# Optimization experiments

Measured on AMD Instinct MI355X. Metric: run time of the kernel, lower is better.

Reference implementation:

```python
import jax, jax.numpy as jnp
import numpy as np


def conv2d(x, w, pad=0, groups=1, bias=None):
    out = jax.lax.conv_general_dilated(
        x, w, (1, 1), [(pad, pad), (pad, pad)],
        dimension_numbers=('NCHW', 'OIHW', 'NCHW'), feature_group_count=groups)
    return out if bias is None else out + bias[None, :, None, None]


def l2norm(t):
    # F.normalize(t, dim=-1): divide by max(||t||_2, 1e-12)
    return t / jnp.maximum(jnp.sqrt(jnp.sum(t * t, axis=-1, keepdims=True)), 1e-12)


def chan_attn(q, k, v, temp, heads):
    # transposed (channel) attention: contract over N=H*W, softmax over small channel dim
    b, _, h, w = v.shape
    n = h * w
    q = l2norm(q.reshape(b, heads, -1, n))
    k = l2norm(k.reshape(b, heads, -1, n))
    v = v.reshape(b, heads, -1, n)
    attn = jax.nn.softmax(jnp.einsum('bhdn,bhen->bhde', q, k) * temp, axis=-1)
    return jnp.einsum('bhde,bhen->bhdn', attn, v).reshape(b, -1, h, w)


def nearest_resize(x, H, W):
    # torch F.interpolate(mode='nearest'): idx = floor(i * in/out)
    hi, wi = x.shape[2], x.shape[3]
    iy = jnp.arange(H) * hi // H
    ix = jnp.arange(W) * wi // W
    return x[:, :, iy][:, :, :, ix]


def deform_conv(x, offsets, w, bias, k, pad, groups):
    # torchvision DeformConv2d, stride=1, dilation=1, offset layout [B, 2*k*k, H, W] as (dy, dx) pairs
    B, Cin, H, W = x.shape
    K2 = k * k
    off = offsets.reshape(B, K2, 2, H, W)
    ky, kx = jnp.meshgrid(jnp.arange(k), jnp.arange(k), indexing='ij')
    py = (jnp.arange(H)[None, None, :, None] - pad) + ky.reshape(1, K2, 1, 1) + off[:, :, 0]
    px = (jnp.arange(W)[None, None, None, :] - pad) + kx.reshape(1, K2, 1, 1) + off[:, :, 1]
    y0f = jnp.floor(py); x0f = jnp.floor(px)
    wy = (py - y0f)[:, None]  # [B,1,K2,H,W]
    wx = (px - x0f)[:, None]
    y0 = y0f.astype(jnp.int32); x0 = x0f.astype(jnp.int32)
    xf = x.reshape(B, Cin, H * W)

    def gather(yi, xi):
        valid = ((yi >= 0) & (yi < H) & (xi >= 0) & (xi < W)).astype(x.dtype)
        idx = (jnp.clip(yi, 0, H - 1) * W + jnp.clip(xi, 0, W - 1)).reshape(B, 1, -1)
        v = jnp.take_along_axis(xf, idx, axis=2).reshape(B, Cin, K2, H, W)
        return v * valid[:, None]

    s = (gather(y0, x0) * (1 - wy) * (1 - wx)
         + gather(y0, x0 + 1) * (1 - wy) * wx
         + gather(y0 + 1, x0) * wy * (1 - wx)
         + gather(y0 + 1, x0 + 1) * wy * wx)  # [B, Cin, K2, H, W]
    g = groups
    s = s.reshape(B, g, Cin // g, K2, H, W)
    wg = w.reshape(g, w.shape[0] // g, Cin // g, K2)
    out = jnp.einsum('bgckhw,gock->bgohw', s, wg).reshape(B, -1, H, W)
    return out + bias[None, :, None, None]


def scconv(x, w_k2, w_k3, w_k4):
    B, C, H, W = x.shape
    p = x.reshape(B, C, H // 2, 2, W // 2, 2).mean(axis=(3, 5))  # AvgPool2d(2,2)
    a = jax.nn.sigmoid(nearest_resize(conv2d(p, w_k2, pad=0), H, W))
    return conv2d(conv2d(x, w_k3, pad=1) * a, w_k4, pad=1)


def layernorm_c(x, g, b):
    # LayerNorm over channel dim of NCHW (applied as [B, HW, C] in the original)
    b_, c, h, w = x.shape
    t = x.reshape(b_, c, h * w).transpose(0, 2, 1)
    mu = t.mean(-1, keepdims=True)
    var = ((t - mu) ** 2).mean(-1, keepdims=True)
    t = (t - mu) / jnp.sqrt(var + 1e-5) * g + b
    return t.transpose(0, 2, 1).reshape(b_, c, h, w)


def _forward(x, y, temp, w_po, w_lp1, w_lp2, ln_g, ln_b, temp_in, w_qkv, w_qkvd,
             w_mproj, w_c3, w_k2, w_k3, w_k4, w_d3, b_d3, w_d5, b_d5, w_d7, b_d7,
             w_pw, b_pw):
    b, c, h, w = x.shape
    heads = 8
    # --- Multi_Receptive_Attentive_Prompts ---
    l1 = conv2d(x, w_lp1)
    l2 = conv2d(x, w_lp2, pad=1)
    xn = layernorm_c(x, ln_g, ln_b)
    qkv = conv2d(conv2d(xn, w_qkv), w_qkvd, pad=1, groups=c)
    qi, ki, vi = jnp.split(qkv, 3, axis=1)
    xg = x + conv2d(chan_attn(qi, ki, vi, temp_in, heads), w_mproj)
    prompt = conv2d(jnp.concatenate([l1, l2, xg], axis=1), w_c3, pad=1)
    # --- Temporal_Alignment ---
    offs = scconv(jnp.concatenate([x, y], axis=1), w_k2, w_k3, w_k4)  # [B,166,H,W]
    f3 = jax.nn.relu(deform_conv(x, offs[:, :18], w_d3, b_d3, 3, 1, 8))
    f5 = jax.nn.relu(deform_conv(x, offs[:, 18:68], w_d5, b_d5, 5, 2, 8))
    f7 = jax.nn.relu(deform_conv(x, offs[:, 68:166], w_d7, b_d7, 7, 3, 8))
    k_feat = conv2d(jnp.concatenate([f3, f5, f7], axis=1), w_pw, bias=b_pw)
    # --- prompted channel attention ---
    q_feat = jnp.concatenate([x, prompt], axis=1)  # 2c channels -> d_q = 2c/heads
    out = chan_attn(q_feat, k_feat, x, temp, heads)  # [B, 2c, H, W]
    return conv2d(out, w_po)


def setup_inputs() -> dict:
    key = jax.random.key(0)
    ks = jax.random.split(key, 16)
    C, B, H, W = 32, 2, 128, 128
    r = lambda k, shp: jax.random.normal(k, shp, dtype=jnp.float32) * 0.05
    return {
        'x': jax.random.normal(ks[0], (B, C, H, W), dtype=jnp.float32),
        'y': jax.random.normal(ks[1], (B, C, H, W), dtype=jnp.float32),
        'temp': jnp.ones((1, 8, 1, 1), jnp.float32),
        'w_po': r(ks[2], (C, 2 * C, 1, 1)),
        'w_lp1': r(ks[3], (C, C, 1, 1)),
        'w_lp2': r(ks[4], (C, C, 3, 3)),
        'ln_g': jnp.ones((C,), jnp.float32),
        'ln_b': jnp.zeros((C,), jnp.float32),
        'temp_in': jnp.ones((1, 8, 1, 1), jnp.float32),
        'w_qkv': r(ks[5], (3 * C, C, 1, 1)),
        'w_qkvd': r(ks[6], (3 * C, 3, 3, 3)),  # groups=C: in/groups = 3
        'w_mproj': r(ks[7], (C, C, 1, 1)),
        'w_c3': r(ks[8], (C, 3 * C, 3, 3)),
        'w_k2': r(ks[9], (166, 2 * C, 3, 3)),
        'w_k3': r(ks[10], (166, 2 * C, 3, 3)),
        'w_k4': r(ks[11], (166, 166, 3, 3)),
        'w_d3': r(ks[12], (C, C // 8, 3, 3)),
        'b_d3': jnp.zeros((C,), jnp.float32),
        'w_d5': r(ks[13], (C, C // 8, 5, 5)),
        'b_d5': jnp.zeros((C,), jnp.float32),
        'w_d7': r(ks[14], (C, C // 8, 7, 7)),
        'b_d7': jnp.zeros((C,), jnp.float32),
        'w_pw': r(ks[15], (C, 3 * C, 1, 1)),
        'b_pw': jnp.zeros((C,), jnp.float32),
    }


def reference(x, y, temp, w_po, w_lp1, w_lp2, ln_g, ln_b, temp_in, w_qkv, w_qkvd,
              w_mproj, w_c3, w_k2, w_k3, w_k4, w_d3, b_d3, w_d5, b_d5, w_d7, b_d7,
              w_pw, b_pw):
    return _forward(x, y, temp, w_po, w_lp1, w_lp2, ln_g, ln_b, temp_in, w_qkv,
                    w_qkvd, w_mproj, w_c3, w_k2, w_k3, w_k4, w_d3, b_d3, w_d5,
                    b_d5, w_d7, b_d7, w_pw, b_pw)
```

## Files before the change

kernel.cpp:

```cpp
#include <hip/hip_runtime.h>
#include <hip/hip_bf16.h>
#include <hip/hip_fp16.h>


constexpr int B = 2, C = 32, H = 128, W = 128, N = H * W;

using bh8   = __attribute__((ext_vector_type(8))) short;
using f32x4 = __attribute__((ext_vector_type(4))) float;

__device__ __forceinline__ ushort f2bf(float v) {
  __hip_bfloat16 h = __float2bfloat16(v);
  return *(ushort*)&h;
}
__device__ __forceinline__ float bf2f(ushort u) {
  union { unsigned int i; float f; } w; w.i = ((unsigned int)u) << 16; return w.f;
}

__global__ __launch_bounds__(256) void k_prep(const float* __restrict__ x,
                                              const float* __restrict__ y,
                                              const float* __restrict__ ln_g,
                                              const float* __restrict__ ln_b,
                                              float* __restrict__ cat2,
                                              ushort* __restrict__ xtb,
                                              ushort* __restrict__ cat2b,
                                              float* __restrict__ xn,
                                              ushort* __restrict__ poolb) {
  __shared__ float tile[C][257];
  const int b = blockIdx.y, n0 = blockIdx.x * 256, tid = threadIdx.x;
  const int n = n0 + tid;
  const int prow = blockIdx.x;
  for (int c = 0; c < C; c++) {
    float v = x[(size_t)(b * C + c) * N + n];
    tile[c][tid] = v;
    cat2[(size_t)(b * 64 + c) * N + n] = v;
  }
  __syncthreads();
  {
    float s = 0.f, ss = 0.f;
#pragma unroll
    for (int c = 0; c < C; c++) { const float v = tile[c][tid]; s += v; ss += v * v; }
    const float mu = s * (1.f / C);
    const float var = ss * (1.f / C) - mu * mu;
    const float inv = rsqrtf(var + 1e-5f);
#pragma unroll
    for (int c = 0; c < C; c++)
      xn[(size_t)(b * C + c) * N + n] = (tile[c][tid] - mu) * inv * ln_g[c] + ln_b[c];
  }
  for (int i = tid; i < C * 256; i += 256) {
    int c = i & 31, nl = i >> 5;
    const ushort bv = f2bf(tile[c][nl]);
    xtb[((size_t)b * N + n0 + nl) * 32 + c] = bv;
    cat2b[((size_t)b * N + n0 + nl) * 64 + c] = bv;
  }
  for (int i = tid; i < 2048; i += 256) {
    const int ox = i >> 5, c = i & 31;
    const float pv = 0.25f * (tile[c][2 * ox] + tile[c][2 * ox + 1]
                            + tile[c][128 + 2 * ox] + tile[c][128 + 2 * ox + 1]);
    poolb[((size_t)b * 4096 + prow * 64 + ox) * 64 + c] = f2bf(pv);
  }
  __syncthreads();
  for (int c = 0; c < C; c++) {
    float v = y[(size_t)(b * C + c) * N + n];
    tile[c][tid] = v;
    cat2[(size_t)(b * 64 + 32 + c) * N + n] = v;
  }
  __syncthreads();
  for (int i = tid; i < C * 256; i += 256) {
    int c = i & 31, nl = i >> 5;
    cat2b[((size_t)b * N + n0 + nl) * 64 + 32 + c] = f2bf(tile[c][nl]);
  }
  for (int i = tid; i < 2048; i += 256) {
    const int ox = i >> 5, c = i & 31;
    const float pv = 0.25f * (tile[c][2 * ox] + tile[c][2 * ox + 1]
                            + tile[c][128 + 2 * ox] + tile[c][128 + 2 * ox + 1]);
    poolb[((size_t)b * 4096 + prow * 64 + ox) * 64 + 32 + c] = f2bf(pv);
  }
}

struct WEnt { const float* src; ushort* dst; int cout_real, cin_real, kc32, total; };
struct WArgs { WEnt e[5]; };

__global__ __launch_bounds__(256) void k_wpack(WArgs a) {
  const WEnt en = a.e[blockIdx.y];
  const int tk = 9 * en.kc32;
  for (int i = blockIdx.x * 256 + threadIdx.x; i < en.total; i += gridDim.x * 256) {
    const int co = i / tk, rem = i - co * tk;
    const int t = rem / en.kc32, ci = rem - t * en.kc32;
    float v = 0.f;
    if (co < en.cout_real && ci < en.cin_real)
      v = en.src[((size_t)co * en.cin_real + ci) * 9 + t];
    en.dst[i] = f2bf(v);
  }
}

__global__ __launch_bounds__(256)
void k_conv3m(const ushort* __restrict__ xin, long in_bs, int in_cs, int ih, int iw,
              const ushort* __restrict__ wp, int kchunks, int cout_real,
              void* __restrict__ outp, long out_bs, int out_coff,
              int oh, int ow, int pad, int omode, int out_cs, int store_tot,
              const float* __restrict__ gatep) {
  __shared__ ushort smem[17408];
  ushort* xt = smem;
  const int tid = threadIdx.x, b = blockIdx.z;
  const int y0 = blockIdx.x * 2, co0 = blockIdx.y * 32;
  const int wv = tid >> 6, lane = tid & 63;
  const int row_sel = wv >> 1, col0 = (wv & 1) * 64;
  const int q = lane >> 4, n = lane & 15, q8 = q * 8;
  const int kc32 = kchunks * 32;
  const ushort* xb = xin + (size_t)b * in_bs;

  f32x4 acc[2][4];
#pragma unroll
  for (int mt = 0; mt < 2; mt++)
#pragma unroll
    for (int nb = 0; nb < 4; nb++) acc[mt][nb] = (f32x4){0.f, 0.f, 0.f, 0.f};

  for (int cc = 0; cc < kchunks; cc++) {
    __syncthreads();
    for (int i = tid; i < 2080; i += 256) {
      const int qq = i & 3, rc = i >> 2;
      const int r = rc / 130, c = rc - r * 130;
      const int yy = y0 - pad + r, xx = c - pad;
      bh8 v = {0, 0, 0, 0, 0, 0, 0, 0};
      if (yy >= 0 && yy < ih && xx >= 0 && xx < iw)
        v = *(const bh8*)(xb + ((size_t)yy * iw + xx) * in_cs + cc * 32 + qq * 8);
      *(bh8*)&xt[rc * 32 + qq * 8] = v;
    }
    __syncthreads();
#pragma unroll
    for (int t = 0; t < 9; t++) {
      const int dy = t / 3, dx = t - dy * 3;
      bh8 a[2], bb[4];
#pragma unroll
      for (int mt = 0; mt < 2; mt++)
        a[mt] = *(const bh8*)(wp + (size_t)((co0 + mt * 16 + n) * 9 + t) * kc32 + cc * 32 + q8);
#pragma unroll
      for (int nb = 0; nb < 4; nb++)
        bb[nb] = *(const bh8*)&xt[((row_sel + dy) * 130 + col0 + nb * 16 + n + dx) * 32 + q8];
#pragma unroll
      for (int mt = 0; mt < 2; mt++)
#pragma unroll
        for (int nb = 0; nb < 4; nb++)
          acc[mt][nb] = __builtin_amdgcn_mfma_f32_16x16x32_bf16(a[mt], bb[nb], acc[mt][nb], 0, 0, 0);
    }
  }

  const size_t osp = (size_t)oh * ow;
  if (omode == 0) {
    const int oy = y0 + row_sel;
    float* ob = (float*)outp + (size_t)b * out_bs + (size_t)out_coff * osp + (size_t)oy * ow;
#pragma unroll
    for (int mt = 0; mt < 2; mt++)
#pragma unroll
      for (int r = 0; r < 4; r++) {
        const int co = co0 + mt * 16 + q * 4 + r;
        if (co < cout_real) {
#pragma unroll
          for (int nb = 0; nb < 4; nb++) {
            const int px = col0 + nb * 16 + n;
            if (px < ow) ob[(size_t)co * osp + px] = acc[mt][nb][r];
          }
        }
      }
  } else if (omode == 1) {
    __syncthreads();
#pragma unroll
    for (int mt = 0; mt < 2; mt++)
#pragma unroll
      for (int nb = 0; nb < 4; nb++) {
        const int px = col0 + nb * 16 + n;
        ushort4 o;
        o.x = f2bf(acc[mt][nb][0]); o.y = f2bf(acc[mt][nb][1]);
        o.z = f2bf(acc[mt][nb][2]); o.w = f2bf(acc[mt][nb][3]);
        *(ushort4*)&smem[(row_sel * 128 + px) * 36 + mt * 16 + q * 4] = o;
      }
    __syncthreads();
    {
      const int row = tid >> 7, px = tid & 127;
      const int oy2 = y0 + row;
      const int sc = min(32, store_tot - co0);
      if (px < ow && sc > 0) {
        ushort* dst = (ushort*)outp + ((size_t)b * osp + (size_t)oy2 * ow + px) * out_cs
                      + out_coff + co0;
        const ushort* src = &smem[(row * 128 + px) * 36];
        if (gatep) {
          const int iy = (oy2 * 62) >> 7, ix2 = (px * 62) >> 7;
          const float* gp = gatep + ((size_t)b * 3844 + iy * 62 + ix2) * 168;
          for (int c = 0; c < sc; c += 4) {
            ushort4 v = *(const ushort4*)(src + c);
            const int ch0 = out_coff + co0 + c;
            float g0 = 1.f, g1 = 1.f, g2 = 1.f, g3 = 1.f;
            if (ch0 + 3 < 166) {
              const float4 a4 = *(const float4*)(gp + ch0);
              g0 = 1.f / (1.f + expf(-a4.x)); g1 = 1.f / (1.f + expf(-a4.y));
              g2 = 1.f / (1.f + expf(-a4.z)); g3 = 1.f / (1.f + expf(-a4.w));
            } else {
              if (ch0 + 0 < 166) g0 = 1.f / (1.f + expf(-gp[ch0 + 0]));
              if (ch0 + 1 < 166) g1 = 1.f / (1.f + expf(-gp[ch0 + 1]));
              if (ch0 + 2 < 166) g2 = 1.f / (1.f + expf(-gp[ch0 + 2]));
              if (ch0 + 3 < 166) g3 = 1.f / (1.f + expf(-gp[ch0 + 3]));
            }
            v.x = f2bf(bf2f(v.x) * g0); v.y = f2bf(bf2f(v.y) * g1);
            v.z = f2bf(bf2f(v.z) * g2); v.w = f2bf(bf2f(v.w) * g3);
            *(ushort4*)(dst + c) = v;
          }
        } else {
          for (int c = 0; c < sc; c += 4)
            *(ushort4*)(dst + c) = *(const ushort4*)(src + c);
        }
      }
    }
  } else {
    float* tf = (float*)smem;
    for (int round = 0; round < 2; round++) {
      __syncthreads();
      if (row_sel == round) {
#pragma unroll
        for (int mt = 0; mt < 2; mt++)
#pragma unroll
          for (int nb = 0; nb < 4; nb++) {
            const int px = col0 + nb * 16 + n;
            *(f32x4*)&tf[px * 34 + mt * 16 + q * 4] = acc[mt][nb];
          }
      }
      __syncthreads();
      const int px = tid & 127, half = tid >> 7;
      const int oy2 = y0 + round;
      if (px < ow) {
        float* dst = (float*)outp + ((size_t)b * osp + (size_t)oy2 * ow + px) * out_cs
                     + out_coff + co0 + half * 16;
        const float* src = &tf[px * 34 + half * 16];
        for (int c = 0; c < 16; c += 4) {
          if (co0 + half * 16 + c + 3 < store_tot)
            *(float4*)(dst + c) = *(const float4*)(src + c);
        }
      }
    }
  }
}

template <int PX>
__global__ __launch_bounds__(256)
void k_conv1x1v(const float* __restrict__ in, long in_bs, int cin,
                const float* __restrict__ wts, const float* __restrict__ bias,
                float* __restrict__ out, long out_bs, int out_coff,
                ushort* __restrict__ outb, int ob_cs) {
  const int n0 = (blockIdx.x * 256 + threadIdx.x) * PX;
  const int co0 = blockIdx.y * 4, b = blockIdx.z;
  const float* ip = in + (size_t)b * in_bs + n0;
  const float* w = wts + (size_t)co0 * cin;
  float acc[4][PX] = {};
  for (int ci = 0; ci < cin; ci++) {
    float xv[PX];
    if (PX == 4) {
      const float4 v = *(const float4*)(ip + (size_t)ci * N);
      xv[0] = v.x; xv[1] = v.y; xv[2] = v.z; xv[3] = v.w;
    } else {
      const float2 v = *(const float2*)(ip + (size_t)ci * N);
      xv[0] = v.x; xv[1] = v.y;
    }
    const float w0 = w[ci], w1 = w[cin + ci], w2 = w[2 * cin + ci], w3 = w[3 * cin + ci];
#pragma unroll
    for (int p = 0; p < PX; p++) {
      acc[0][p] += xv[p] * w0; acc[1][p] += xv[p] * w1;
      acc[2][p] += xv[p] * w2; acc[3][p] += xv[p] * w3;
    }
  }
  if (bias) {
#pragma unroll
    for (int o = 0; o < 4; o++) {
      const float bv = bias[co0 + o];
#pragma unroll
      for (int p = 0; p < PX; p++) acc[o][p] += bv;
    }
  }
  if (outb) {
#pragma unroll
    for (int p = 0; p < PX; p++) {
      ushort4 o;
      o.x = f2bf(acc[0][p]); o.y = f2bf(acc[1][p]);
      o.z = f2bf(acc[2][p]); o.w = f2bf(acc[3][p]);
      *(ushort4*)(outb + ((size_t)b * N + n0 + p) * ob_cs + out_coff + co0) = o;
    }
  } else {
#pragma unroll
    for (int o = 0; o < 4; o++) {
      if (PX == 4)
        *(float4*)(out + (size_t)b * out_bs + (size_t)(out_coff + co0 + o) * N + n0) =
            make_float4(acc[o][0], acc[o][1], acc[o][2], acc[o][3]);
      else
        *(float2*)(out + (size_t)b * out_bs + (size_t)(out_coff + co0 + o) * N + n0) =
            make_float2(acc[o][0], acc[o][1]);
    }
  }
}

__global__ __launch_bounds__(256) void k_dwconv(const float* __restrict__ in,
                                                const float* __restrict__ wts,
                                                float* __restrict__ out) {
  const int n0 = (blockIdx.x * 256 + threadIdx.x) * 4;
  const int g = blockIdx.y, b = blockIdx.z;
  const int h0 = n0 >> 7, w0 = n0 & 127;
  float acc[3][4] = {};
  for (int ci = 0; ci < 3; ci++) {
    const float* ip = in + ((size_t)b * 96 + g * 3 + ci) * N;
    float v[3][6];
#pragma unroll
    for (int r = 0; r < 3; r++) {
      const int iy = h0 - 1 + r;
      const bool rowok = (iy >= 0) & (iy < H);
#pragma unroll
      for (int j = 0; j < 6; j++) {
        const int ix = w0 - 1 + j;
        v[r][j] = (rowok && ix >= 0 && ix < W) ? ip[(size_t)iy * W + ix] : 0.f;
      }
    }
#pragma unroll
    for (int o = 0; o < 3; o++) {
      const float* wp = wts + ((size_t)(g * 3 + o) * 3 + ci) * 9;
#pragma unroll
      for (int r = 0; r < 3; r++) {
        const float wa = wp[r * 3 + 0], wb = wp[r * 3 + 1], wc = wp[r * 3 + 2];
#pragma unroll
        for (int p = 0; p < 4; p++)
          acc[o][p] += v[r][p] * wa + v[r][p + 1] * wb + v[r][p + 2] * wc;
      }
    }
  }
#pragma unroll
  for (int o = 0; o < 3; o++)
    *(float4*)(out + ((size_t)b * 96 + g * 3 + o) * N + n0) =
        make_float4(acc[o][0], acc[o][1], acc[o][2], acc[o][3]);
}

template <int DQ>
__global__ __launch_bounds__(256)
void k_attn_part(const float* __restrict__ q1, long q1_bs,
                 const float* __restrict__ q2, long q2_bs,
                 const float* __restrict__ k, long k_bs,
                 float* __restrict__ partial) {
  const int h = blockIdx.x, b = blockIdx.y, ch = blockIdx.z, tid = threadIdx.x;
  const float* qp[DQ];
#pragma unroll
  for (int d = 0; d < DQ; d++) {
    const int qc = h * DQ + d;
    qp[d] = (qc < 32) ? (q1 + (size_t)b * q1_bs + (size_t)qc * N)
                      : (q2 + (size_t)b * q2_bs + (size_t)(qc - 32) * N);
  }
  const float* kp[4];
#pragma unroll
  for (int e = 0; e < 4; e++) kp[e] = k + (size_t)b * k_bs + (size_t)(h * 4 + e) * N;

  constexpr int NV = DQ + 4 + DQ * 4;
  float ssq[DQ] = {}, ssk[4] = {}, gr[DQ][4] = {};
  const int n1 = (ch + 1) * (N / 16);
  for (int n = ch * (N / 16) + tid; n < n1; n += 256) {
    float qv[DQ], kv[4];
#pragma unroll
    for (int d = 0; d < DQ; d++) { qv[d] = qp[d][n]; ssq[d] += qv[d] * qv[d]; }
#pragma unroll
    for (int e = 0; e < 4; e++) { kv[e] = kp[e][n]; ssk[e] += kv[e] * kv[e]; }
#pragma unroll
    for (int d = 0; d < DQ; d++)
#pragma unroll
      for (int e = 0; e < 4; e++) gr[d][e] += qv[d] * kv[e];
  }
  float vals[NV];
#pragma unroll
  for (int d = 0; d < DQ; d++) vals[d] = ssq[d];
#pragma unroll
  for (int e = 0; e < 4; e++) vals[DQ + e] = ssk[e];
#pragma unroll
  for (int d = 0; d < DQ; d++)
#pragma unroll
    for (int e = 0; e < 4; e++) vals[DQ + 4 + d * 4 + e] = gr[d][e];
#pragma unroll
  for (int j = 0; j < NV; j++) {
    float v = vals[j];
    for (int m = 32; m > 0; m >>= 1) v += __shfl_xor(v, m, 64);
    vals[j] = v;
  }
  __shared__ float red[4][NV];
  const int wid = tid >> 6, lane = tid & 63;
  if (lane == 0)
#pragma unroll
    for (int j = 0; j < NV; j++) red[wid][j] = vals[j];
  __syncthreads();
  if (tid < NV)
    partial[(size_t)(((b * 8 + h) * 16) + ch) * NV + tid] =
        red[0][tid] + red[1][tid] + red[2][tid] + red[3][tid];
}

template <int DQ>
__global__ __launch_bounds__(128)
void k_attn_soft(const float* __restrict__ partial,
                 const float* __restrict__ temp, float* __restrict__ stats) {
  constexpr int NV = DQ + 4 + DQ * 4;
  const int h = blockIdx.x, b = blockIdx.y, tid = threadIdx.x;
  __shared__ float tot[NV];
  if (tid < NV) {
    float s = 0.f;
#pragma unroll
    for (int ch = 0; ch < 16; ch++)
      s += partial[(size_t)(((b * 8 + h) * 16) + ch) * NV + tid];
    tot[tid] = s;
  }
  __syncthreads();
  if (tid == 0) {
    float invq[DQ], invk[4];
#pragma unroll
    for (int d = 0; d < DQ; d++) invq[d] = 1.f / fmaxf(sqrtf(tot[d]), 1e-12f);
#pragma unroll
    for (int e = 0; e < 4; e++) invk[e] = 1.f / fmaxf(sqrtf(tot[DQ + e]), 1e-12f);
    const float t = temp[h];
    float* sp = stats + (size_t)(b * 8 + h) * DQ * 4;
    for (int d = 0; d < DQ; d++) {
      float s[4], mx = -1e30f;
#pragma unroll
      for (int e = 0; e < 4; e++) {
        s[e] = tot[DQ + 4 + d * 4 + e] * invq[d] * invk[e] * t;
        mx = fmaxf(mx, s[e]);
      }
      float sum = 0.f;
#pragma unroll
      for (int e = 0; e < 4; e++) { s[e] = expf(s[e] - mx); sum += s[e]; }
#pragma unroll
      for (int e = 0; e < 4; e++) sp[d * 4 + e] = s[e] / sum;
    }
  }
}

template <int DQ>
__global__ __launch_bounds__(256)
void k_fold(const float* __restrict__ stats, const float* __restrict__ w,
            float* __restrict__ M) {
  const int b = blockIdx.x;
  for (int idx = threadIdx.x; idx < 1024; idx += 256) {
    const int co = idx >> 5, j = idx & 31;
    const int h = j >> 2, e = j & 3;
    const float* A = stats + ((size_t)b * 8 + h) * DQ * 4;
    const float* wr = w + co * (8 * DQ) + h * DQ;
    float s = 0.f;
#pragma unroll
    for (int d = 0; d < DQ; d++) s += wr[d] * A[d * 4 + e];
    M[((size_t)b * 32 + co) * 32 + j] = s;
  }
}

__global__ __launch_bounds__(256)
void k_attn_mproj2(const float* __restrict__ qkv2, const float* __restrict__ M2,
                   const float* __restrict__ x, ushort* __restrict__ cat1b) {
  __shared__ float mls[512];
  const int tid = threadIdx.x, b = blockIdx.y, z = blockIdx.z;
  const int n = blockIdx.x * 256 + tid;
  for (int i = tid; i < 512; i += 256)
    mls[i] = M2[((size_t)b * 32 + z * 16) * 32 + i];
  __syncthreads();
  const float* vi = qkv2 + (size_t)b * (96L * N) + 64L * N;
  float vv[32];
#pragma unroll
  for (int ci = 0; ci < 32; ci++) vv[ci] = vi[(size_t)ci * N + n];
  ushort to[16];
  for (int o = 0; o < 16; o++) {
    const float* m = &mls[o * 32];
    float r = 0.f;
#pragma unroll
    for (int ci = 0; ci < 32; ci += 4) {
      const float4 w4 = *(const float4*)&m[ci];
      r += w4.x * vv[ci] + w4.y * vv[ci + 1] + w4.z * vv[ci + 2] + w4.w * vv[ci + 3];
    }
    r += x[(size_t)(b * 64 + z * 16 + o) * N + n];
    to[o] = f2bf(r);
  }
  ushort* dp = cat1b + ((size_t)b * N + n) * 96 + 64 + z * 16;
#pragma unroll
  for (int k = 0; k < 2; k++) *(bh8*)(dp + k * 8) = *(const bh8*)&to[k * 8];
}

__global__ __launch_bounds__(256)
void k_attn_po2(const float* __restrict__ cat2, const float* __restrict__ M,
                float* __restrict__ outp) {
  __shared__ float mls[512];
  const int tid = threadIdx.x, b = blockIdx.y, z = blockIdx.z;
  const int n = blockIdx.x * 256 + tid;
  for (int i = tid; i < 512; i += 256)
    mls[i] = M[((size_t)b * 32 + z * 16) * 32 + i];
  __syncthreads();
  const float* v = cat2 + (size_t)b * (64L * N);
  float vv[32];
#pragma unroll
  for (int ci = 0; ci < 32; ci++) vv[ci] = v[(size_t)ci * N + n];
  for (int o = 0; o < 16; o++) {
    const float* m = &mls[o * 32];
    float r = 0.f;
#pragma unroll
    for (int ci = 0; ci < 32; ci += 4) {
      const float4 w4 = *(const float4*)&m[ci];
      r += w4.x * vv[ci] + w4.y * vv[ci + 1] + w4.z * vv[ci + 2] + w4.w * vv[ci + 3];
    }
    outp[(size_t)(b * 32 + z * 16 + o) * N + n] = r;
  }
}

__global__ __launch_bounds__(256)
void k_deform7(const ushort* __restrict__ xtb, const float* __restrict__ offs,
               const float* __restrict__ wd3, const float* __restrict__ bd3,
               const float* __restrict__ wd5, const float* __restrict__ bd5,
               const float* __restrict__ wd7, const float* __restrict__ bd7,
               float* __restrict__ out) {
  const int tid = threadIdx.x, b = blockIdx.y;
  const int zone = blockIdx.x >> 9;
  const int blk = blockIdx.x & 511;
  int K, off_c0, out_c0;
  const float *wd, *bd;
  if (zone == 0)      { K = 3; off_c0 = 0;  out_c0 = 0;  wd = wd3; bd = bd3; }
  else if (zone == 1) { K = 5; off_c0 = 18; out_c0 = 32; wd = wd5; bd = bd5; }
  else                { K = 7; off_c0 = 68; out_c0 = 64; wd = wd7; bd = bd7; }
  const int K2 = K * K, PAD = K / 2;

  extern __shared__ __align__(16) char smem[];
  __half*  wlds = (__half*)smem;
  __half*  wbl  = wlds + K2 * 128;
  ushort*  abl  = (ushort*)(wbl + 32 * K2 * 4);

  for (int i = tid; i < K2 * 128; i += 256) {
    const int t = i >> 7, r = i & 127;
    const int g = r >> 4, oo = (r >> 2) & 3, ci = r & 3;
    wlds[i] = __float2half(wd[(size_t)((g * 4 + oo) * 4 + ci) * K2 + t]);
  }
  const int px0 = blk * 32;
  const float* obb = offs + ((size_t)b * N) * 168;
  for (int i = tid; i < 32 * K2; i += 256) {
    const int p = i / K2, t = i - p * K2;
    const int px = px0 + p;
    const int hy = px >> 7, wx = px & 127;
    const int ky = t / K, kx = t - ky * K;
    const float* ob2 = obb + (size_t)px * 168 + off_c0;
    const float dy = ob2[2 * t];
    const float dx = ob2[2 * t + 1];
    const float py = (float)(hy - PAD + ky) + dy;
    const float pxf = (float)(wx - PAD + kx) + dx;
    const float y0f = floorf(py), x0f = floorf(pxf);
    const float fy = py - y0f, fx = pxf - x0f;
    const int y0 = (int)y0f, x0 = (int)x0f;
    const int y1 = y0 + 1, x1 = x0 + 1;
    float w00 = (1.f - fy) * (1.f - fx), w01 = (1.f - fy) * fx;
    float w10 = fy * (1.f - fx), w11 = fy * fx;
    const bool vy0 = (y0 >= 0) & (y0 < H), vy1 = (y1 >= 0) & (y1 < H);
    const bool vx0 = (x0 >= 0) & (x0 < W), vx1 = (x1 >= 0) & (x1 < W);
    w00 = (vy0 & vx0) ? w00 : 0.f;
    w01 = (vy0 & vx1) ? w01 : 0.f;
    w10 = (vy1 & vx0) ? w10 : 0.f;
    w11 = (vy1 & vx1) ? w11 : 0.f;
    const int cy0 = min(max(y0, 0), H - 1), cy1 = min(max(y1, 0), H - 1);
    const int cx0 = min(max(x0, 0), W - 1), cx1 = min(max(x1, 0), W - 1);
    const int base = (p * K2 + t) * 4;
    wbl[base + 0] = __float2half(w00); wbl[base + 1] = __float2half(w01);
    wbl[base + 2] = __float2half(w10); wbl[base + 3] = __float2half(w11);
    abl[base + 0] = (ushort)(cy0 * W + cx0);
    abl[base + 1] = (ushort)(cy0 * W + cx1);
    abl[base + 2] = (ushort)(cy1 * W + cx0);
    abl[base + 3] = (ushort)(cy1 * W + cx1);
  }
  __syncthreads();

  const int pxl = tid >> 3, g = tid & 7;
  const int px = px0 + pxl;
  const ushort* xb = xtb + (size_t)b * N * 32 + g * 4;
  float acc[4] = {0.f, 0.f, 0.f, 0.f};
  for (int t = 0; t < K2; t++) {
    const int base = (pxl * K2 + t) * 4;
    const ushort4 r4 = *(const ushort4*)&abl[base];
    const float2 w01v = __half22float2(*(const __half2*)&wbl[base]);
    const float2 w23v = __half22float2(*(const __half2*)&wbl[base + 2]);
    const ushort4 c0 = *(const ushort4*)(xb + (size_t)r4.x * 32);
    const ushort4 c1 = *(const ushort4*)(xb + (size_t)r4.y * 32);
    const ushort4 c2 = *(const ushort4*)(xb + (size_t)r4.z * 32);
    const ushort4 c3 = *(const ushort4*)(xb + (size_t)r4.w * 32);
    const float s0 = w01v.x * bf2f(c0.x) + w01v.y * bf2f(c1.x)
                   + w23v.x * bf2f(c2.x) + w23v.y * bf2f(c3.x);
    const float s1 = w01v.x * bf2f(c0.y) + w01v.y * bf2f(c1.y)
                   + w23v.x * bf2f(c2.y) + w23v.y * bf2f(c3.y);
    const float s2 = w01v.x * bf2f(c0.z) + w01v.y * bf2f(c1.z)
                   + w23v.x * bf2f(c2.z) + w23v.y * bf2f(c3.z);
    const float s3 = w01v.x * bf2f(c0.w) + w01v.y * bf2f(c1.w)
                   + w23v.x * bf2f(c2.w) + w23v.y * bf2f(c3.w);
    const __half2* wp2 = (const __half2*)&wlds[(t * 8 + g) * 16];
#pragma unroll
    for (int oo = 0; oo < 4; oo++) {
      const float2 u01 = __half22float2(wp2[oo * 2]);
      const float2 u23 = __half22float2(wp2[oo * 2 + 1]);
      acc[oo] += s0 * u01.x + s1 * u01.y + s2 * u23.x + s3 * u23.y;
    }
  }
#pragma unroll
  for (int oo = 0; oo < 4; oo++) {
    const float r = fmaxf(acc[oo] + bd[g * 4 + oo], 0.f);
    out[((size_t)b * 96 + out_c0 + g * 4 + oo) * N + px] = r;
  }
}

extern "C" void kernel_launch(void* const* d_in, const int* in_sizes, int n_in,
                              void* d_out, int out_size, void* d_ws, size_t ws_size,
                              hipStream_t stream) {
  const float* fx       = (const float*)d_in[0];
  const float* fy       = (const float*)d_in[1];
  const float* w_temp   = (const float*)d_in[2];
  const float* w_po     = (const float*)d_in[3];
  const float* w_lp1    = (const float*)d_in[4];
  const float* w_lp2    = (const float*)d_in[5];
  const float* ln_g     = (const float*)d_in[6];
  const float* ln_b     = (const float*)d_in[7];
  const float* w_tempin = (const float*)d_in[8];
  const float* w_qkv    = (const float*)d_in[9];
  const float* w_qkvd   = (const float*)d_in[10];
  const float* w_mproj  = (const float*)d_in[11];
  const float* w_c3     = (const float*)d_in[12];
  const float* w_k2     = (const float*)d_in[13];
  const float* w_k3     = (const float*)d_in[14];
  const float* w_k4     = (const float*)d_in[15];
  const float* w_d3     = (const float*)d_in[16];
  const float* b_d3     = (const float*)d_in[17];
  const float* w_d5     = (const float*)d_in[18];
  const float* b_d5     = (const float*)d_in[19];
  const float* w_d7     = (const float*)d_in[20];
  const float* b_d7     = (const float*)d_in[21];
  const float* w_pw     = (const float*)d_in[22];
  const float* b_pw     = (const float*)d_in[23];
  float* ws = (float*)d_ws;

  size_t off = 0;
  auto buf = [&](size_t nelem) { float* p = ws + off; off += nelem; return p; };
  float* CAT2   = buf(2097152);
  float* XTBf   = buf(1048576);
  float* R1     = buf(1048576);
  float* R2     = buf(3145728);
  float* R3     = buf(3145728);
  float* PROMPT = buf(1048576);
  float* R4     = buf(5439488);
  float* OFFS   = buf(5505024);
  float* STATS  = buf(65536);
  float* CAT2Bf = buf(524288);
  float* WPf    = buf(327680);
  float* POOLBf = buf(262144);
  (void)ws_size; (void)out_size; (void)n_in; (void)in_sizes;

  float* XN = R1;
  float* QKV1 = R2;
  float* QKV2 = R3;   float* ASMALL = R3 + 524288;
  float* CAT3 = R4;   float* KFEAT = R4 + 3145728;
  float* ST_IN = STATS;
  float* ST_FI = STATS + 256;
  float* M_IN  = STATS + 1024;
  float* M_FI  = STATS + 3072;
  float* P_IN  = STATS + 5120;
  float* P_FI  = STATS + 14336;

  ushort* XTb   = (ushort*)XTBf;
  ushort* CAT2b = (ushort*)CAT2Bf;
  ushort* POOLb = (ushort*)POOLBf;
  ushort* CAT1b = (ushort*)OFFS;
  ushort* T3b   = (ushort*)R2;

  ushort* WPu = (ushort*)WPf;
  ushort* wp_lp2 = WPu;
  ushort* wp_c3  = wp_lp2 + 18432;
  ushort* wp_k2  = wp_c3 + 55296;
  ushort* wp_k3  = wp_k2 + 110592;
  ushort* wp_k4  = wp_k3 + 110592;

  const long bs64 = 64L * N, bs32 = 32L * N, bs96 = 96L * N;

  WArgs wa;
  wa.e[0] = { w_lp2, wp_lp2, 32, 32, 32, 64 * 9 * 32 };
  wa.e[1] = { w_c3,  wp_c3,  32, 96, 96, 64 * 9 * 96 };
  wa.e[2] = { w_k2,  wp_k2, 166, 64, 64, 192 * 9 * 64 };
  wa.e[3] = { w_k3,  wp_k3, 166, 64, 64, 192 * 9 * 64 };
  wa.e[4] = { w_k4,  wp_k4, 166, 166, 192, 192 * 9 * 192 };
  k_wpack<<<dim3(64, 5), 256, 0, stream>>>(wa);
  k_prep<<<dim3(N / 256, B), 256, 0, stream>>>(
      fx, fy, ln_g, ln_b, CAT2, XTb, CAT2b, XN, POOLb);
  k_conv1x1v<4><<<dim3(N / 1024, 24, B), 256, 0, stream>>>(
      XN, bs32, 32, w_qkv, nullptr, QKV1, bs96, 0, nullptr, 0);
  k_dwconv<<<dim3(N / 1024, 32, B), 256, 0, stream>>>(QKV1, w_qkvd, QKV2);
  k_attn_part<4><<<dim3(8, B, 16), 256, 0, stream>>>(
      QKV2, bs96, nullptr, 0, QKV2 + bs32, bs96, P_IN);
  k_attn_soft<4><<<dim3(8, B), 128, 0, stream>>>(P_IN, w_tempin, ST_IN);
  k_fold<4><<<dim3(B), 256, 0, stream>>>(ST_IN, w_mproj, M_IN);
  k_attn_mproj2<<<dim3(N / 256, B, 2), 256, 0, stream>>>(QKV2, M_IN, CAT2, CAT1b);
  k_conv1x1v<2><<<dim3(N / 512, 8, B), 256, 0, stream>>>(
      CAT2, bs64, 32, w_lp1, nullptr, nullptr, 0, 0, CAT1b, 96);
  k_conv3m<<<dim3(64, 1, B), 256, 0, stream>>>(
      CAT2b, (long)N * 64, 64, H, W, wp_lp2, 1, 32, CAT1b, 0, 32, H, W, 1, 1, 96, 32,
      nullptr);
  k_conv3m<<<dim3(64, 1, B), 256, 0, stream>>>(
      CAT1b, (long)N * 96, 96, H, W, wp_c3, 3, 32, PROMPT, bs32, 0, H, W, 1, 0, 0, 0,
      nullptr);
  k_conv3m<<<dim3(31, 6, B), 256, 0, stream>>>(
      POOLb, 4096L * 64, 64, 64, 64, wp_k2, 2, 166, ASMALL, 0, 0, 62, 62, 0, 2, 168, 168,
      nullptr);
  k_conv3m<<<dim3(64, 6, B), 256, 0, stream>>>(
      CAT2b, (long)N * 64, 64, H, W, wp_k3, 2, 166, T3b, 0, 0, H, W, 1, 1, 192, 192,
      ASMALL);
  k_conv3m<<<dim3(64, 6, B), 256, 0, stream>>>(
      T3b, (long)N * 192, 192, H, W, wp_k4, 6, 166, OFFS, 0, 0, H, W, 1, 2, 168, 168,
      nullptr);
  {
    const int K2m = 49;
    const size_t smem = (size_t)K2m * 128 * 2 + (size_t)32 * K2m * 4 * 2 * 2;
    k_deform7<<<dim3(3 * (N / 32), B), 256, smem, stream>>>(
        XTb, OFFS, w_d3, b_d3, w_d5, b_d5, w_d7, b_d7, CAT3);
  }
  k_conv1x1v<2><<<dim3(N / 512, 8, B), 256, 0, stream>>>(
      CAT3, bs96, 96, w_pw, b_pw, KFEAT, bs32, 0, nullptr, 0);
  k_attn_part<8><<<dim3(8, B, 16), 256, 0, stream>>>(
      CAT2, bs64, PROMPT, bs32, KFEAT, bs32, P_FI);
  k_attn_soft<8><<<dim3(8, B), 128, 0, stream>>>(P_FI, w_temp, ST_FI);
  k_fold<8><<<dim3(B), 256, 0, stream>>>(ST_FI, w_po, M_FI);
  k_attn_po2<<<dim3(N / 256, B, 2), 256, 0, stream>>>(CAT2, M_FI, (float*)d_out);
}
```

Measured before the change: 441.3 us.

## Run 1x1 convs as bf16 MFMA GEMMs on channel-last bf16 activations

The layernorm output and the deformable-conv output are now written as channel-last bf16 instead of channel-first fp32. Both 1x1 convolutions (the qkv projection and the pointwise fuse) move from the fp32 vector kernel to a new MFMA 16x16x32 bf16 GEMM kernel, with their weights cast to bf16 by a small extra kernel. This halves intermediate memory traffic and uses matrix cores. The cost is extra bf16 rounding of activations and weights, plus one more launch.

```diff
diff --git a/kernel.cpp b/kernel.cpp
--- a/kernel.cpp
+++ b/kernel.cpp
@@ -23,7 +23,7 @@
                                               float* __restrict__ cat2,
                                               ushort* __restrict__ xtb,
                                               ushort* __restrict__ cat2b,
-                                              float* __restrict__ xn,
+                                              ushort* __restrict__ xnb,
                                               ushort* __restrict__ poolb) {
   __shared__ float tile[C][257];
   const int b = blockIdx.y, n0 = blockIdx.x * 256, tid = threadIdx.x;
@@ -42,9 +42,13 @@
     const float mu = s * (1.f / C);
     const float var = ss * (1.f / C) - mu * mu;
     const float inv = rsqrtf(var + 1e-5f);
+    ushort xo[32];
 #pragma unroll
     for (int c = 0; c < C; c++)
-      xn[(size_t)(b * C + c) * N + n] = (tile[c][tid] - mu) * inv * ln_g[c] + ln_b[c];
+      xo[c] = f2bf((tile[c][tid] - mu) * inv * ln_g[c] + ln_b[c]);
+    ushort* dp = xnb + ((size_t)b * N + n) * 32;
+#pragma unroll
+    for (int k = 0; k < 4; k++) *(bh8*)(dp + k * 8) = *(const bh8*)&xo[k * 8];
   }
   for (int i = tid; i < C * 256; i += 256) {
     int c = i & 31, nl = i >> 5;
@@ -91,6 +95,46 @@
       v = en.src[((size_t)co * en.cin_real + ci) * 9 + t];
     en.dst[i] = f2bf(v);
   }
+}
+
+__global__ __launch_bounds__(256)
+void k_castw(const float* __restrict__ a, ushort* __restrict__ da, int na,
+             const float* __restrict__ b2, ushort* __restrict__ db, int nb2) {
+  const int i = blockIdx.x * 256 + threadIdx.x;
+  if (i < na) da[i] = f2bf(a[i]);
+  if (i < nb2) db[i] = f2bf(b2[i]);
+}
+
+template <int MT, int KC>
+__global__ __launch_bounds__(256)
+void k_gemm1x1(const ushort* __restrict__ in, int in_cs,
+               const ushort* __restrict__ wq, const float* __restrict__ bias,
+               float* __restrict__ out, long out_bs) {
+  const int tid = threadIdx.x, b = blockIdx.y;
+  const int px0 = blockIdx.x * 64 + (tid >> 6) * 16;
+  const int lane = tid & 63, q = lane >> 4, n = lane & 15, q8 = q * 8;
+  f32x4 acc[MT];
+#pragma unroll
+  for (int mt = 0; mt < MT; mt++) acc[mt] = (f32x4){0.f, 0.f, 0.f, 0.f};
+  const ushort* ib = in + (size_t)b * N * in_cs;
+#pragma unroll
+  for (int kc = 0; kc < KC; kc++) {
+    const bh8 bb = *(const bh8*)(ib + (size_t)(px0 + n) * in_cs + kc * 32 + q8);
+#pragma unroll
+    for (int mt = 0; mt < MT; mt++) {
+      const bh8 a = *(const bh8*)(wq + (size_t)(mt * 16 + n) * (KC * 32) + kc * 32 + q8);
+      acc[mt] = __builtin_amdgcn_mfma_f32_16x16x32_bf16(a, bb, acc[mt], 0, 0, 0);
+    }
+  }
+  float* ob = out + (size_t)b * out_bs;
+#pragma unroll
+  for (int mt = 0; mt < MT; mt++)
+#pragma unroll
+    for (int r = 0; r < 4; r++) {
+      const int co = mt * 16 + q * 4 + r;
+      const float bv = bias ? bias[co] : 0.f;
+      ob[(size_t)co * N + px0 + n] = acc[mt][r] + bv;
+    }
 }
 
 __global__ __launch_bounds__(256)
@@ -507,7 +551,7 @@
                const float* __restrict__ wd3, const float* __restrict__ bd3,
                const float* __restrict__ wd5, const float* __restrict__ bd5,
                const float* __restrict__ wd7, const float* __restrict__ bd7,
-               float* __restrict__ out) {
+               ushort* __restrict__ cat3b) {
   const int tid = threadIdx.x, b = blockIdx.y;
   const int zone = blockIdx.x >> 9;
   const int blk = blockIdx.x & 511;
@@ -593,11 +637,12 @@
       acc[oo] += s0 * u01.x + s1 * u01.y + s2 * u23.x + s3 * u23.y;
     }
   }
-#pragma unroll
-  for (int oo = 0; oo < 4; oo++) {
-    const float r = fmaxf(acc[oo] + bd[g * 4 + oo], 0.f);
-    out[((size_t)b * 96 + out_c0 + g * 4 + oo) * N + px] = r;
-  }
+  ushort4 o;
+  o.x = f2bf(fmaxf(acc[0] + bd[g * 4 + 0], 0.f));
+  o.y = f2bf(fmaxf(acc[1] + bd[g * 4 + 1], 0.f));
+  o.z = f2bf(fmaxf(acc[2] + bd[g * 4 + 2], 0.f));
+  o.w = f2bf(fmaxf(acc[3] + bd[g * 4 + 3], 0.f));
+  *(ushort4*)(cat3b + ((size_t)b * N + px) * 96 + out_c0 + g * 4) = o;
 }
 
 extern "C" void kernel_launch(void* const* d_in, const int* in_sizes, int n_in,
@@ -645,10 +690,9 @@
   float* POOLBf = buf(262144);
   (void)ws_size; (void)out_size; (void)n_in; (void)in_sizes;
 
-  float* XN = R1;
   float* QKV1 = R2;
   float* QKV2 = R3;   float* ASMALL = R3 + 524288;
-  float* CAT3 = R4;   float* KFEAT = R4 + 3145728;
+  float* KFEAT = R4 + 3145728;
   float* ST_IN = STATS;
   float* ST_FI = STATS + 256;
   float* M_IN  = STATS + 1024;
@@ -657,9 +701,11 @@
   float* P_FI  = STATS + 14336;
 
   ushort* XTb   = (ushort*)XTBf;
+  ushort* XNb   = (ushort*)R1;
   ushort* CAT2b = (ushort*)CAT2Bf;
   ushort* POOLb = (ushort*)POOLBf;
   ushort* CAT1b = (ushort*)OFFS;
+  ushort* CAT3b = (ushort*)R4;
   ushort* T3b   = (ushort*)R2;
 
   ushort* WPu = (ushort*)WPf;
@@ -668,6 +714,8 @@
   ushort* wp_k2  = wp_c3 + 55296;
   ushort* wp_k3  = wp_k2 + 110592;
   ushort* wp_k4  = wp_k3 + 110592;
+  ushort* wq_qkv = wp_k4 + 331776;
+  ushort* wq_pw  = wq_qkv + 3072;
 
   const long bs64 = 64L * N, bs32 = 32L * N, bs96 = 96L * N;
 
@@ -678,10 +726,11 @@
   wa.e[3] = { w_k3,  wp_k3, 166, 64, 64, 192 * 9 * 64 };
   wa.e[4] = { w_k4,  wp_k4, 166, 166, 192, 192 * 9 * 192 };
   k_wpack<<<dim3(64, 5), 256, 0, stream>>>(wa);
+  k_castw<<<dim3(12), 256, 0, stream>>>(w_qkv, wq_qkv, 3072, w_pw, wq_pw, 3072);
   k_prep<<<dim3(N / 256, B), 256, 0, stream>>>(
-      fx, fy, ln_g, ln_b, CAT2, XTb, CAT2b, XN, POOLb);
-  k_conv1x1v<4><<<dim3(N / 1024, 24, B), 256, 0, stream>>>(
-      XN, bs32, 32, w_qkv, nullptr, QKV1, bs96, 0, nullptr, 0);
+      fx, fy, ln_g, ln_b, CAT2, XTb, CAT2b, XNb, POOLb);
+  k_gemm1x1<6, 1><<<dim3(N / 64, B), 256, 0, stream>>>(
+      XNb, 32, wq_qkv, nullptr, QKV1, bs96);
   k_dwconv<<<dim3(N / 1024, 32, B), 256, 0, stream>>>(QKV1, w_qkvd, QKV2);
   k_attn_part<4><<<dim3(8, B, 16), 256, 0, stream>>>(
       QKV2, bs96, nullptr, 0, QKV2 + bs32, bs96, P_IN);
@@ -709,10 +758,10 @@
     const int K2m = 49;
     const size_t smem = (size_t)K2m * 128 * 2 + (size_t)32 * K2m * 4 * 2 * 2;
     k_deform7<<<dim3(3 * (N / 32), B), 256, smem, stream>>>(
-        XTb, OFFS, w_d3, b_d3, w_d5, b_d5, w_d7, b_d7, CAT3);
-  }
-  k_conv1x1v<2><<<dim3(N / 512, 8, B), 256, 0, stream>>>(
-      CAT3, bs96, 96, w_pw, b_pw, KFEAT, bs32, 0, nullptr, 0);
+        XTb, OFFS, w_d3, b_d3, w_d5, b_d5, w_d7, b_d7, CAT3b);
+  }
+  k_gemm1x1<2, 3><<<dim3(N / 64, B), 256, 0, stream>>>(
+      CAT3b, 96, wq_pw, b_pw, KFEAT, bs32);
   k_attn_part<8><<<dim3(8, B, 16), 256, 0, stream>>>(
       CAT2, bs64, PROMPT, bs32, KFEAT, bs32, P_FI);
   k_attn_soft<8><<<dim3(8, B), 128, 0, stream>>>(P_FI, w_temp, ST_FI);
```

Result: faster. 409.1 us (-7.3%).
